# Optimization experiments

Measured on AMD Instinct MI355X. Metric: run time of the kernel, lower is better.

The kernel has to match this reference:

```python
import jax, jax.numpy as jnp
import numpy as np

B, N, D = 8, 2048, 1024
DC = 1024          # d_center
K = 4              # num_centers
NUM_JUMPS = 2
SPAN = 2
FIN = (2 + 2 * NUM_JUMPS + 1) * D  # 7*D

def _gelu(x):
    return jax.nn.gelu(x, approximate=False)  # torch nn.GELU default is exact erf

def setup_inputs() -> dict:
    key = jax.random.key(0)
    ks = jax.random.split(key, 16)
    s = lambda k, *sh: jax.random.normal(k, sh, dtype=jnp.float32) * 0.02
    return {
        "queries": jax.random.normal(ks[0], (B, N, D), dtype=jnp.float32),
        "fr_w1": s(ks[1], FIN, D), "fr_b1": jnp.zeros((D,), jnp.float32),
        "fr_w2": s(ks[2], D, D),   "fr_b2": jnp.zeros((D,), jnp.float32),
        "tc_w1": s(ks[3], D, DC),  "tc_b1": jnp.zeros((DC,), jnp.float32),
        "tc_w2": s(ks[4], DC, DC), "tc_b2": jnp.zeros((DC,), jnp.float32),
        "centers": jax.random.normal(ks[5], (K, DC), dtype=jnp.float32),
        "fc_w1": s(ks[6], D + DC, D), "fc_b1": jnp.zeros((D,), jnp.float32),
        "fc_w2": s(ks[7], D, D),      "fc_b2": jnp.zeros((D,), jnp.float32),
        "g_w": s(ks[8], D + DC, D),   "g_b": jnp.zeros((D,), jnp.float32),
    }

def reference(queries, fr_w1, fr_b1, fr_w2, fr_b2,
              tc_w1, tc_b1, tc_w2, tc_b2, centers,
              fc_w1, fc_b1, fc_w2, fc_b2, g_w, g_b):
    x = queries
    shifts = [1, -1, 0]  # left, right, x
    for i in range(1, NUM_JUMPS + 1):
        shifts += [i * SPAN, -i * SPAN]
    fusion = jnp.concatenate([jnp.roll(x, s, axis=1) for s in shifts], axis=-1)  # [B,N,7D]
    x_ring = _gelu(fusion @ fr_w1 + fr_b1) @ fr_w2 + fr_b2                       # [B,N,D]
    token_proj = _gelu(x_ring @ tc_w1 + tc_b1) @ tc_w2 + tc_b2                   # [B,N,DC]
    w = jax.nn.softmax(jnp.einsum('bnd,kd->bnk', token_proj, centers), axis=-1)  # [B,N,K]
    weighted = jnp.einsum('bnk,kd->bnd', w, centers)                             # [B,N,DC]
    fus2 = jnp.concatenate([x_ring, weighted], axis=-1)                          # [B,N,D+DC]
    gate = jax.nn.sigmoid(fus2 @ g_w + g_b)
    fc = _gelu(fus2 @ fc_w1 + fc_b1) @ fc_w2 + fc_b2
    return gate * fc + (1.0 - gate) * x_ring
```

## Files before the change

### kernel.cpp

```cpp
#include <hip/hip_runtime.h>
#include <hip/hip_bf16.h>
#include <math.h>

typedef unsigned short u16;
typedef __attribute__((ext_vector_type(8))) short short8;
typedef __attribute__((ext_vector_type(4))) float f32x4;


__device__ __forceinline__ float bf2f(u16 b) {
  return __uint_as_float(((unsigned int)b) << 16);
}
__device__ __forceinline__ u16 f2bf(float f) {
  unsigned int u = __float_as_uint(f);
  u += 0x7FFFu + ((u >> 16) & 1u);
  return (u16)(u >> 16);
}
__device__ __forceinline__ float gelu_exact(float x) {
  return 0.5f * x * (1.0f + erff(x * 0.70710678118654752f));
}

__device__ __forceinline__ void cp16(const void* g, void* l) {
  __builtin_amdgcn_global_load_lds(
      (const __attribute__((address_space(1))) unsigned int*)g,
      (__attribute__((address_space(3))) unsigned int*)l, 16, 0, 0);
}

template <int MODE, bool GATHER>
__global__ __launch_bounds__(512) void gemm256(
    const u16* __restrict__ A, int lda, const u16* __restrict__ Wt, int K,
    const float* __restrict__ bias, const float* __restrict__ bias2,
    void* __restrict__ out0, int ldo0, void* __restrict__ out1,
    void* __restrict__ out2, const float* __restrict__ p0,
    const float* __restrict__ p1, const float* __restrict__ p2) {
  extern __shared__ __align__(16) char sm[];
  const int tid = threadIdx.x;
  const int lane = tid & 63;
  const int wave = tid >> 6;
  const int wm = wave >> 2;
  const int wn = wave & 3;

  const unsigned linear = blockIdx.y * gridDim.x + blockIdx.x;
  const unsigned xcd = linear & 7u;
  const unsigned pos = linear >> 3;
  const unsigned bx = pos % gridDim.x;
  const unsigned by = xcd * (gridDim.y >> 3) + pos / gridDim.x;
  const int m0 = by * 256;
  const int n0 = bx * 256;

  const int sl = lane >> 3;
  const int qqs = (lane & 7) ^ sl;
  const int rowoff = sl * 2 + (qqs >> 2);
  const int colq = qqs & 3;

  const int r16 = lane & 15, q4 = lane >> 4;
  const int qqr = (((r16 & 1) << 2) | q4) ^ (r16 >> 1);
  const int laneA = wm * 8192 + (r16 >> 1) * 128 + qqr * 16;
  const int laneB = wn * 4096 + (r16 >> 1) * 128 + qqr * 16;

  const int nt = K >> 5;

  f32x4 acc[8][4];
#pragma unroll
  for (int i = 0; i < 8; i++)
#pragma unroll
    for (int j = 0; j < 4; j++) acc[i][j] = (f32x4){0.f, 0.f, 0.f, 0.f};

  auto stage_A = [&](int sdst, int ssrc) {
#pragma unroll
    for (int i = 0; i < 2; i++) {
      const int chunk = wave + i * 8;
      const int row = chunk * 16 + rowoff;
      long gofs;
      if (GATHER) {
        const int kg = ssrc * 32 + colq * 8;
        const int seg = kg >> 10;
        int shift;
        switch (seg) {
          case 0: shift = 1; break;
          case 1: shift = -1; break;
          case 2: shift = 0; break;
          case 3: shift = 2; break;
          case 4: shift = -2; break;
          case 5: shift = 4; break;
          default: shift = -4; break;
        }
        const int m = m0 + row;
        const int b = m >> 11;
        const int nsrc = ((m & 2047) - shift) & 2047;
        gofs = (long)((b << 11) | nsrc) * 1024 + (kg & 1023);
      } else {
        gofs = (long)(m0 + row) * lda + ssrc * 32 + colq * 8;
      }
      cp16(A + gofs, sm + (sdst & 3) * 32768 + chunk * 1024);
    }
  };
  auto stage_B = [&](int sdst, int ssrc) {
#pragma unroll
    for (int i = 0; i < 2; i++) {
      const int chunk = wave + i * 8;
      const int row = chunk * 16 + rowoff;
      const long gofs = (long)(n0 + row) * K + ssrc * 32 + colq * 8;
      cp16(Wt + gofs, sm + (sdst & 3) * 32768 + 16384 + chunk * 1024);
    }
  };

  stage_A(0, 0); stage_B(0, 0);
  stage_A(1, 1); stage_B(1, 1);

  for (int s = 0; s < nt; ++s) {
    const int s2 = (s + 2 < nt) ? s + 2 : nt - 1;
    stage_A(s + 2, s2);
    stage_B(s + 2, s2);
    asm volatile("s_waitcnt vmcnt(4)" ::: "memory");
    __builtin_amdgcn_s_barrier();

    const char* abase = sm + (s & 3) * 32768;
    short8 af[8], bf[4];
#pragma unroll
    for (int ni = 0; ni < 4; ni++)
      bf[ni] = *(const short8*)(abase + 16384 + laneB + ni * 1024);
#pragma unroll
    for (int mi = 0; mi < 8; mi++)
      af[mi] = *(const short8*)(abase + laneA + mi * 1024);

    asm volatile("s_waitcnt lgkmcnt(4)" ::: "memory");
    __builtin_amdgcn_sched_barrier(0);
    __builtin_amdgcn_s_setprio(1);
#pragma unroll
    for (int mi = 0; mi < 4; mi++)
#pragma unroll
      for (int ni = 0; ni < 4; ni++)
        acc[mi][ni] = __builtin_amdgcn_mfma_f32_16x16x32_bf16(
            af[mi], bf[ni], acc[mi][ni], 0, 0, 0);
    __builtin_amdgcn_s_setprio(0);

    asm volatile("s_waitcnt lgkmcnt(0)" ::: "memory");
    __builtin_amdgcn_sched_barrier(0);
    __builtin_amdgcn_s_setprio(1);
#pragma unroll
    for (int mi = 0; mi < 4; mi++)
#pragma unroll
      for (int ni = 0; ni < 4; ni++)
        acc[4 + mi][ni] = __builtin_amdgcn_mfma_f32_16x16x32_bf16(
            af[4 + mi], bf[ni], acc[4 + mi][ni], 0, 0, 0);
    __builtin_amdgcn_s_setprio(0);
  }
  asm volatile("s_waitcnt vmcnt(0)" ::: "memory");

  const int ccol = lane & 15;
  const int crow = (lane >> 4) * 4;
#pragma unroll
  for (int mi = 0; mi < 8; mi++) {
#pragma unroll
    for (int r = 0; r < 4; r++) {
      const int m = m0 + wm * 128 + mi * 16 + crow + r;
      float4 wrow;
      if (MODE == 8) wrow = *(const float4*)(p0 + (size_t)m * 4);
#pragma unroll
      for (int ni = 0; ni < 4; ni++) {
        const int n = n0 + wn * 64 + ni * 16 + ccol;
        const float v = acc[mi][ni][r];
        if (MODE == 0) {
          ((u16*)out0)[(long)m * ldo0 + n] = f2bf(gelu_exact(v + bias[n]));
        } else if (MODE == 4) {
          const float g = p0[(long)m * 1024 + n];
          const float xr = p1[(long)m * 1024 + n];
          ((float*)out0)[(long)m * ldo0 + n] =
              g * (v + bias[n]) + (1.0f - g) * xr;
        } else if (MODE == 6) {
          ((u16*)out0)[(long)m * ldo0 + n] = f2bf(v);
        } else if (MODE == 7) {
          if (n < 1024) {
            const float s = v + bias[n];
            ((float*)out1)[(long)m * 1024 + n] = s;
            ((u16*)out0)[(long)m * 1024 + n] = f2bf(s);
          } else {
            const int nn = n - 1024;
            ((u16*)out2)[(long)m * 1024 + nn] = f2bf(gelu_exact(v + bias2[nn]));
          }
        } else if (MODE == 8) {
          if (n < 1024) {
            const float4 g2 = *(const float4*)(p1 + (size_t)n * 4);
            const float s = v + bias[n] + wrow.x * g2.x + wrow.y * g2.y +
                            wrow.z * g2.z + wrow.w * g2.w;
            ((float*)out0)[(long)m * 1024 + n] = 1.0f / (1.0f + expf(-s));
          } else {
            const int nn = n - 1024;
            const float4 f2 = *(const float4*)(p2 + (size_t)nn * 4);
            const float s = v + bias2[nn] + wrow.x * f2.x + wrow.y * f2.y +
                            wrow.z * f2.z + wrow.w * f2.w;
            ((u16*)out1)[(long)m * 1024 + nn] = f2bf(gelu_exact(s));
          }
        }
      }
    }
  }
}

template <int MODE, bool GATHER>
__global__ __launch_bounds__(256) void gemm128(
    const u16* __restrict__ A, int lda, const u16* __restrict__ Wt, int K,
    const float* __restrict__ bias, const float* __restrict__ bias2,
    void* __restrict__ out0, int ldo0, void* __restrict__ out1,
    void* __restrict__ out2, const float* __restrict__ p0,
    const float* __restrict__ p1, const float* __restrict__ p2) {
  __shared__ __align__(16) u16 As[128 * 64];
  __shared__ __align__(16) u16 Bs[128 * 64];

  const int tid = threadIdx.x;
  const int lane = tid & 63;
  const int wave = tid >> 6;
  const int wm = wave >> 1;
  const int wn = wave & 1;

  const unsigned linear = blockIdx.y * gridDim.x + blockIdx.x;
  const unsigned xcd = linear & 7u;
  const unsigned pos = linear >> 3;
  const unsigned bx = pos % gridDim.x;
  const unsigned by = xcd * (gridDim.y >> 3) + pos / gridDim.x;
  const int m0 = by * 128;
  const int n0 = bx * 128;

  const int srow = lane >> 3;
  const int sq = lane & 7;
  const int sqs = sq ^ srow;

  f32x4 acc[4][4];
#pragma unroll
  for (int i = 0; i < 4; i++)
#pragma unroll
    for (int j = 0; j < 4; j++) acc[i][j] = (f32x4){0.f, 0.f, 0.f, 0.f};

  for (int k0 = 0; k0 < K; k0 += 64) {
#pragma unroll
    for (int i = 0; i < 4; i++) {
      const int rloc = wave * 32 + i * 8 + srow;
      long gofs;
      if (GATHER) {
        const int seg = k0 >> 10;
        int shift;
        switch (seg) {
          case 0: shift = 1; break;
          case 1: shift = -1; break;
          case 2: shift = 0; break;
          case 3: shift = 2; break;
          case 4: shift = -2; break;
          case 5: shift = 4; break;
          default: shift = -4; break;
        }
        const int m = m0 + rloc;
        const int b = m >> 11;
        const int nsrc = ((m & 2047) - shift) & 2047;
        gofs = (long)((b << 11) | nsrc) * 1024 + (k0 & 1023) + sqs * 8;
      } else {
        gofs = (long)(m0 + rloc) * lda + k0 + sqs * 8;
      }
      cp16(A + gofs, &As[(wave * 32 + i * 8) * 64]);
    }
#pragma unroll
    for (int i = 0; i < 4; i++) {
      const int rloc = wave * 32 + i * 8 + srow;
      const long gofs = (long)(n0 + rloc) * K + k0 + sqs * 8;
      cp16(Wt + gofs, &Bs[(wave * 32 + i * 8) * 64]);
    }
    __syncthreads();

    const int q4 = lane >> 4;
    const int r16 = lane & 15;
#pragma unroll
    for (int kk = 0; kk < 2; kk++) {
      short8 af[4], bf[4];
#pragma unroll
      for (int mi = 0; mi < 4; mi++) {
        const int row = wm * 64 + mi * 16 + r16;
        const int q = (kk * 4 + q4) ^ (row & 7);
        af[mi] = *(const short8*)&As[row * 64 + q * 8];
      }
#pragma unroll
      for (int ni = 0; ni < 4; ni++) {
        const int row = wn * 64 + ni * 16 + r16;
        const int q = (kk * 4 + q4) ^ (row & 7);
        bf[ni] = *(const short8*)&Bs[row * 64 + q * 8];
      }
#pragma unroll
      for (int mi = 0; mi < 4; mi++)
#pragma unroll
        for (int ni = 0; ni < 4; ni++)
          acc[mi][ni] = __builtin_amdgcn_mfma_f32_16x16x32_bf16(
              af[mi], bf[ni], acc[mi][ni], 0, 0, 0);
    }
    __syncthreads();
  }

  const int ccol = lane & 15;
  const int crow = (lane >> 4) * 4;
#pragma unroll
  for (int mi = 0; mi < 4; mi++) {
#pragma unroll
    for (int r = 0; r < 4; r++) {
      const int m = m0 + wm * 64 + mi * 16 + crow + r;
#pragma unroll
      for (int ni = 0; ni < 4; ni++) {
        const int n = n0 + wn * 64 + ni * 16 + ccol;
        const float v = acc[mi][ni][r];
        if (MODE == 6) {
          ((u16*)out0)[(long)m * ldo0 + n] = f2bf(v);
        }
      }
    }
  }
}

__global__ __launch_bounds__(256) void cast_bf16(const float* __restrict__ in,
                                                 u16* __restrict__ out, int n4) {
  const long i = (long)blockIdx.x * 256 + threadIdx.x;
  if (i < n4) {
    const float4 v = ((const float4*)in)[i];
    ushort4 o;
    o.x = f2bf(v.x); o.y = f2bf(v.y); o.z = f2bf(v.z); o.w = f2bf(v.w);
    ((ushort4*)out)[i] = o;
  }
}

__global__ __launch_bounds__(256) void transp_bf16(const float* __restrict__ in,
                                                   u16* __restrict__ out, int K,
                                                   int N) {
  __shared__ float tile[32][33];
  const int tx = threadIdx.x & 31;
  const int ty = threadIdx.x >> 5;
  const long r0 = (long)blockIdx.y * 32;
  const long c0 = (long)blockIdx.x * 32;
#pragma unroll
  for (int r = 0; r < 4; r++)
    tile[ty + r * 8][tx] = in[(r0 + ty + r * 8) * N + c0 + tx];
  __syncthreads();
#pragma unroll
  for (int r = 0; r < 4; r++)
    out[(c0 + ty + r * 8) * K + r0 + tx] = f2bf(tile[tx][ty + r * 8]);
}

__global__ __launch_bounds__(256) void fold_all(
    const u16* __restrict__ GbT, const u16* __restrict__ FbT,
    const u16* __restrict__ Wt3, const float* __restrict__ centers,
    const float* __restrict__ fr_b2, const float* __restrict__ tc_b1,
    const float* __restrict__ tc_w2, const float* __restrict__ tc_b2,
    float* __restrict__ G2T, float* __restrict__ F2T, float* __restrict__ c2,
    float* __restrict__ S, float* __restrict__ bc) {
  const int b = blockIdx.x;
  const int wave = threadIdx.x >> 6, lane = threadIdx.x & 63;
  if (b < 256) {
    const int n = b * 4 + wave;
    float g[4] = {0.f, 0.f, 0.f, 0.f}, f[4] = {0.f, 0.f, 0.f, 0.f};
#pragma unroll
    for (int p = 0; p < 2; p++) {
      const int base = p * 512 + lane * 8;
      const short8 gv = *(const short8*)(GbT + (long)n * 1024 + base);
      const short8 fv = *(const short8*)(FbT + (long)n * 1024 + base);
#pragma unroll
      for (int e = 0; e < 8; e++) {
        const float ge = bf2f((u16)gv[e]), fe = bf2f((u16)fv[e]);
#pragma unroll
        for (int k = 0; k < 4; k++) {
          const float c = centers[k * 1024 + base + e];
          g[k] += ge * c;
          f[k] += fe * c;
        }
      }
    }
#pragma unroll
    for (int k = 0; k < 4; k++)
#pragma unroll
      for (int off = 32; off > 0; off >>= 1) {
        g[k] += __shfl_xor(g[k], off);
        f[k] += __shfl_xor(f[k], off);
      }
    if (lane == 0) {
#pragma unroll
      for (int k = 0; k < 4; k++) {
        G2T[n * 4 + k] = g[k];
        F2T[n * 4 + k] = f[k];
      }
    }
  } else if (b < 512) {
    const int j = (b - 256) * 4 + wave;
    float s = 0.f;
#pragma unroll
    for (int p = 0; p < 2; p++) {
      const int base = p * 512 + lane * 8;
      const short8 wv = *(const short8*)(Wt3 + (long)j * 1024 + base);
#pragma unroll
      for (int e = 0; e < 8; e++) s += fr_b2[base + e] * bf2f((u16)wv[e]);
    }
#pragma unroll
    for (int off = 32; off > 0; off >>= 1) s += __shfl_xor(s, off);
    if (lane == 0) c2[j] = s + tc_b1[j];
  } else if (b < 768) {
    const int d = (b - 512) * 4 + wave;
    const float* row = tc_w2 + (long)d * 1024;
    float s0 = 0.f, s1 = 0.f, s2 = 0.f, s3 = 0.f;
    for (int e = lane; e < 1024; e += 64) {
      const float w = row[e];
      s0 += w * centers[e];
      s1 += w * centers[1024 + e];
      s2 += w * centers[2048 + e];
      s3 += w * centers[3072 + e];
    }
#pragma unroll
    for (int off = 32; off > 0; off >>= 1) {
      s0 += __shfl_xor(s0, off);
      s1 += __shfl_xor(s1, off);
      s2 += __shfl_xor(s2, off);
      s3 += __shfl_xor(s3, off);
    }
    if (lane == 0) {
      S[d] = s0; S[1024 + d] = s1; S[2048 + d] = s2; S[3072 + d] = s3;
    }
  } else {
    const int k = wave;
    float s = 0.f;
    for (int e = lane; e < 1024; e += 64) s += tc_b2[e] * centers[k * 1024 + e];
#pragma unroll
    for (int off = 32; off > 0; off >>= 1) s += __shfl_xor(s, off);
    if (lane == 0) bc[k] = s;
  }
}

__global__ __launch_bounds__(256) void centers_kernel(
    const u16* __restrict__ h2, const float* __restrict__ S,
    const float* __restrict__ bc, float* __restrict__ wtok) {
  const int lane = threadIdx.x & 63;
  const int wave = threadIdx.x >> 6;
  const long t = (long)blockIdx.x * 4 + wave;
  const u16* row = h2 + t * 1024;
  float d0 = 0.f, d1 = 0.f, d2 = 0.f, d3 = 0.f;
#pragma unroll
  for (int j = 0; j < 2; j++) {
    const int dbase = j * 512 + lane * 8;
    const short8 v = *(const short8*)(row + dbase);
#pragma unroll
    for (int e = 0; e < 8; e++) {
      const float x = bf2f((u16)v[e]);
      const int d = dbase + e;
      d0 += x * S[d];
      d1 += x * S[1024 + d];
      d2 += x * S[2048 + d];
      d3 += x * S[3072 + d];
    }
  }
#pragma unroll
  for (int off = 32; off > 0; off >>= 1) {
    d0 += __shfl_xor(d0, off);
    d1 += __shfl_xor(d1, off);
    d2 += __shfl_xor(d2, off);
    d3 += __shfl_xor(d3, off);
  }
  if (lane == 0) {
    d0 += bc[0]; d1 += bc[1]; d2 += bc[2]; d3 += bc[3];
    const float mx = fmaxf(fmaxf(d0, d1), fmaxf(d2, d3));
    float e0 = expf(d0 - mx), e1 = expf(d1 - mx), e2 = expf(d2 - mx),
          e3 = expf(d3 - mx);
    const float inv = 1.0f / (e0 + e1 + e2 + e3);
    *(float4*)(wtok + t * 4) = (float4){e0 * inv, e1 * inv, e2 * inv, e3 * inv};
  }
}

extern "C" void kernel_launch(void* const* d_in, const int* in_sizes, int n_in,
                              void* d_out, int out_size, void* d_ws,
                              size_t ws_size, hipStream_t stream) {
  const float* queries = (const float*)d_in[0];
  const float* fr_w1 = (const float*)d_in[1];
  const float* fr_b1 = (const float*)d_in[2];
  const float* fr_w2 = (const float*)d_in[3];
  const float* fr_b2 = (const float*)d_in[4];
  const float* tc_w1 = (const float*)d_in[5];
  const float* tc_b1 = (const float*)d_in[6];
  const float* tc_w2 = (const float*)d_in[7];
  const float* tc_b2 = (const float*)d_in[8];
  const float* centers = (const float*)d_in[9];
  const float* fc_w1 = (const float*)d_in[10];
  const float* fc_b1 = (const float*)d_in[11];
  const float* fc_w2 = (const float*)d_in[12];
  const float* fc_b2 = (const float*)d_in[13];
  const float* g_w = (const float*)d_in[14];
  const float* g_b = (const float*)d_in[15];

  char* ws = (char*)d_ws;
  u16* Wt1 = (u16*)ws; ws += (size_t)7168 * 1024 * 2;
  u16* Wt3 = (u16*)ws; ws += (size_t)1024 * 1024 * 2;
  u16* Wt6 = (u16*)ws; ws += (size_t)1024 * 1024 * 2;
  u16* WtJ = (u16*)ws; ws += (size_t)2048 * 1024 * 2;
  u16* WtG2 = (u16*)ws; ws += (size_t)2048 * 1024 * 2;
  u16* Fw2b = (u16*)ws; ws += (size_t)1024 * 1024 * 2;
  u16* GbT = (u16*)ws; ws += (size_t)1024 * 1024 * 2;
  u16* FbT = (u16*)ws; ws += (size_t)1024 * 1024 * 2;
  u16* Xb = (u16*)ws;  ws += (size_t)16384 * 1024 * 2;
  u16* h1 = (u16*)ws;  ws += (size_t)16384 * 1024 * 2;
  u16* xrb = (u16*)ws; ws += (size_t)16384 * 1024 * 2;
  float* xring = (float*)ws; ws += (size_t)16384 * 1024 * 4;
  float* wtok = (float*)ws; ws += (size_t)16384 * 4 * 4;
  float* S = (float*)ws; ws += (size_t)4 * 1024 * 4;
  float* G2T = (float*)ws; ws += (size_t)1024 * 4 * 4;
  float* F2T = (float*)ws; ws += (size_t)1024 * 4 * 4;
  float* c2 = (float*)ws; ws += (size_t)1024 * 4;
  float* bc = (float*)ws; ws += 16;
  float* gate = (float*)d_out;
  float* out = (float*)d_out;

  static bool attr_set = false;
  if (!attr_set) {
    attr_set = true;
    (void)hipFuncSetAttribute((const void*)gemm256<0, true>,
                              hipFuncAttributeMaxDynamicSharedMemorySize,
                              131072);
    (void)hipFuncSetAttribute((const void*)gemm256<7, false>,
                              hipFuncAttributeMaxDynamicSharedMemorySize,
                              131072);
    (void)hipFuncSetAttribute((const void*)gemm256<8, false>,
                              hipFuncAttributeMaxDynamicSharedMemorySize,
                              131072);
    (void)hipFuncSetAttribute((const void*)gemm256<4, false>,
                              hipFuncAttributeMaxDynamicSharedMemorySize,
                              131072);
  }

  cast_bf16<<<16384, 256, 0, stream>>>(queries, Xb, 16384 * 1024 / 4);
  cast_bf16<<<1024, 256, 0, stream>>>(fr_w2, Fw2b, 1024 * 1024 / 4);
  transp_bf16<<<dim3(32, 224), 256, 0, stream>>>(fr_w1, Wt1, 7168, 1024);
  transp_bf16<<<dim3(32, 32), 256, 0, stream>>>(tc_w1, Wt3, 1024, 1024);
  transp_bf16<<<dim3(32, 32), 256, 0, stream>>>(fc_w2, Wt6, 1024, 1024);
  transp_bf16<<<dim3(32, 32), 256, 0, stream>>>(fr_w2, WtJ, 1024, 1024);
  transp_bf16<<<dim3(32, 32), 256, 0, stream>>>(g_w, WtG2, 1024, 1024);
  transp_bf16<<<dim3(32, 32), 256, 0, stream>>>(fc_w1,
                                                WtG2 + (size_t)1024 * 1024,
                                                1024, 1024);
  transp_bf16<<<dim3(32, 32), 256, 0, stream>>>(g_w + (size_t)1024 * 1024, GbT,
                                                1024, 1024);
  transp_bf16<<<dim3(32, 32), 256, 0, stream>>>(fc_w1 + (size_t)1024 * 1024,
                                                FbT, 1024, 1024);
  fold_all<<<769, 256, 0, stream>>>(GbT, FbT, Wt3, centers, fr_b2, tc_b1,
                                    tc_w2, tc_b2, G2T, F2T, c2, S, bc);
  gemm128<6, false><<<dim3(8, 8), 256, 0, stream>>>(
      Wt3, 1024, Fw2b, 1024, nullptr, nullptr, WtJ + (size_t)1024 * 1024, 1024,
      nullptr, nullptr, nullptr, nullptr, nullptr);

  gemm256<0, true><<<dim3(4, 64), 512, 131072, stream>>>(
      Xb, 0, Wt1, 7168, fr_b1, nullptr, h1, 1024, nullptr, nullptr, nullptr,
      nullptr, nullptr);
  gemm256<7, false><<<dim3(8, 64), 512, 131072, stream>>>(
      h1, 1024, WtJ, 1024, fr_b2, c2, xrb, 1024, xring, Xb, nullptr, nullptr,
      nullptr);
  centers_kernel<<<4096, 256, 0, stream>>>(Xb, S, bc, wtok);
  gemm256<8, false><<<dim3(8, 64), 512, 131072, stream>>>(
      xrb, 1024, WtG2, 1024, g_b, fc_b1, gate, 1024, h1, nullptr, wtok, G2T,
      F2T);
  gemm256<4, false><<<dim3(4, 64), 512, 131072, stream>>>(
      h1, 1024, Wt6, 1024, fc_b2, nullptr, out, 1024, nullptr, nullptr, gate,
      xring, nullptr);
}
```

Baseline: 810.6 us.

## Deepen GEMM pipeline to 3-stage prefetch with cross-iteration LDS fragment prefetch

After: 795.7 us. About the same (-1.8%).

```diff
diff --git a/kernel.cpp b/kernel.cpp
--- a/kernel.cpp
+++ b/kernel.cpp
@@ -104,48 +104,84 @@
     }
   };
 
+  auto prefetch = [&](int s, short8 (&pbf)[4], short8 (&paf01)[2]) {
+    const char* base = sm + (s & 3) * 32768;
+#pragma unroll
+    for (int ni = 0; ni < 4; ni++)
+      pbf[ni] = *(const short8*)(base + 16384 + laneB + ni * 1024);
+#pragma unroll
+    for (int mi = 0; mi < 2; mi++)
+      paf01[mi] = *(const short8*)(base + laneA + mi * 1024);
+  };
+
+  auto body = [&](int s, short8 (&cbf)[4], short8 (&caf01)[2],
+                  short8 (&nbf)[4], short8 (&naf01)[2]) {
+    const int s3c = (s + 3 < nt) ? s + 3 : nt - 1;
+    stage_A(s + 3, s3c);
+    stage_B(s + 3, s3c);
+    const char* abase = sm + (s & 3) * 32768;
+    short8 afr[6];
+#pragma unroll
+    for (int j = 0; j < 6; j++)
+      afr[j] = *(const short8*)(abase + laneA + (j + 2) * 1024);
+    prefetch(s + 1, nbf, naf01);
+
+    asm volatile("s_waitcnt lgkmcnt(12)" ::: "memory");
+    __builtin_amdgcn_sched_barrier(0);
+    __builtin_amdgcn_s_setprio(1);
+#pragma unroll
+    for (int mi = 0; mi < 2; mi++)
+#pragma unroll
+      for (int ni = 0; ni < 4; ni++)
+        acc[mi][ni] = __builtin_amdgcn_mfma_f32_16x16x32_bf16(
+            caf01[mi], cbf[ni], acc[mi][ni], 0, 0, 0);
+
+    asm volatile("s_waitcnt lgkmcnt(10)" ::: "memory");
+    __builtin_amdgcn_sched_barrier(0);
+#pragma unroll
+    for (int j = 0; j < 2; j++)
+#pragma unroll
+      for (int ni = 0; ni < 4; ni++)
+        acc[2 + j][ni] = __builtin_amdgcn_mfma_f32_16x16x32_bf16(
+            afr[j], cbf[ni], acc[2 + j][ni], 0, 0, 0);
+
+    asm volatile("s_waitcnt lgkmcnt(8)" ::: "memory");
+    __builtin_amdgcn_sched_barrier(0);
+#pragma unroll
+    for (int j = 0; j < 2; j++)
+#pragma unroll
+      for (int ni = 0; ni < 4; ni++)
+        acc[4 + j][ni] = __builtin_amdgcn_mfma_f32_16x16x32_bf16(
+            afr[2 + j], cbf[ni], acc[4 + j][ni], 0, 0, 0);
+
+    asm volatile("s_waitcnt lgkmcnt(6)" ::: "memory");
+    __builtin_amdgcn_sched_barrier(0);
+#pragma unroll
+    for (int j = 0; j < 2; j++)
+#pragma unroll
+      for (int ni = 0; ni < 4; ni++)
+        acc[6 + j][ni] = __builtin_amdgcn_mfma_f32_16x16x32_bf16(
+            afr[4 + j], cbf[ni], acc[6 + j][ni], 0, 0, 0);
+    __builtin_amdgcn_s_setprio(0);
+
+    asm volatile("s_waitcnt vmcnt(4)" ::: "memory");
+    __builtin_amdgcn_s_barrier();
+  };
+
   stage_A(0, 0); stage_B(0, 0);
   stage_A(1, 1); stage_B(1, 1);
-
-  for (int s = 0; s < nt; ++s) {
-    const int s2 = (s + 2 < nt) ? s + 2 : nt - 1;
-    stage_A(s + 2, s2);
-    stage_B(s + 2, s2);
-    asm volatile("s_waitcnt vmcnt(4)" ::: "memory");
-    __builtin_amdgcn_s_barrier();
-
-    const char* abase = sm + (s & 3) * 32768;
-    short8 af[8], bf[4];
-#pragma unroll
-    for (int ni = 0; ni < 4; ni++)
-      bf[ni] = *(const short8*)(abase + 16384 + laneB + ni * 1024);
-#pragma unroll
-    for (int mi = 0; mi < 8; mi++)
-      af[mi] = *(const short8*)(abase + laneA + mi * 1024);
-
-    asm volatile("s_waitcnt lgkmcnt(4)" ::: "memory");
-    __builtin_amdgcn_sched_barrier(0);
-    __builtin_amdgcn_s_setprio(1);
-#pragma unroll
-    for (int mi = 0; mi < 4; mi++)
-#pragma unroll
-      for (int ni = 0; ni < 4; ni++)
-        acc[mi][ni] = __builtin_amdgcn_mfma_f32_16x16x32_bf16(
-            af[mi], bf[ni], acc[mi][ni], 0, 0, 0);
-    __builtin_amdgcn_s_setprio(0);
-
-    asm volatile("s_waitcnt lgkmcnt(0)" ::: "memory");
-    __builtin_amdgcn_sched_barrier(0);
-    __builtin_amdgcn_s_setprio(1);
-#pragma unroll
-    for (int mi = 0; mi < 4; mi++)
-#pragma unroll
-      for (int ni = 0; ni < 4; ni++)
-        acc[4 + mi][ni] = __builtin_amdgcn_mfma_f32_16x16x32_bf16(
-            af[4 + mi], bf[ni], acc[4 + mi][ni], 0, 0, 0);
-    __builtin_amdgcn_s_setprio(0);
-  }
-  asm volatile("s_waitcnt vmcnt(0)" ::: "memory");
+  stage_A(2, 2); stage_B(2, 2);
+  asm volatile("s_waitcnt vmcnt(4)" ::: "memory");
+  __builtin_amdgcn_s_barrier();
+
+  short8 bfA[4], afA[2], bfB[4], afB[2];
+  prefetch(0, bfA, afA);
+
+  for (int s = 0; s < nt; s += 2) {
+    body(s, bfA, afA, bfB, afB);
+    body(s + 1, bfB, afB, bfA, afA);
+  }
+  asm volatile("s_waitcnt vmcnt(0) lgkmcnt(0)" ::: "memory");
 
   const int ccol = lane & 15;
   const int crow = (lane >> 4) * 4;
```
